# Optimization experiments

Measured on AMD Instinct MI355X. Metric: run time of the kernel, lower is better.

The kernel has to match this reference:

```python
import jax, jax.numpy as jnp
import numpy as np

N_NODES = 100000
N_EDGES = 1600000
N_GRAPHS = 64
BN_EPS = 1e-5


def setup_inputs() -> dict:
    key = jax.random.key(0)
    ks = jax.random.split(key, 16)
    inp = {
        'x': jax.random.normal(ks[0], (N_NODES, 768), dtype=jnp.float32),
        'edge_index': jax.random.randint(ks[1], (2, N_EDGES), 0, N_NODES, dtype=jnp.int32),
        'batch': jnp.sort(jax.random.randint(ks[2], (N_NODES,), 0, N_GRAPHS, dtype=jnp.int32)),
        'W_in': jax.random.normal(ks[3], (768, 256), dtype=jnp.float32) * 0.02,
        'b_in': jax.random.normal(ks[4], (256,), dtype=jnp.float32) * 0.02,
        'W_g': jax.random.normal(ks[5], (3, 256, 256), dtype=jnp.float32) * 0.05,
        'b_g': jax.random.normal(ks[6], (3, 256), dtype=jnp.float32) * 0.02,
        'bn_gamma': jax.random.uniform(ks[7], (3, 256), dtype=jnp.float32) + 0.5,
        'bn_beta': jax.random.normal(ks[8], (3, 256), dtype=jnp.float32) * 0.02,
        'bn_mean': jax.random.normal(ks[9], (3, 256), dtype=jnp.float32) * 0.02,
        'bn_var': jax.random.uniform(ks[10], (3, 256), dtype=jnp.float32) + 0.5,
        'W1': jax.random.normal(ks[11], (256, 128), dtype=jnp.float32) * 0.06,
        'b1': jax.random.normal(ks[12], (128,), dtype=jnp.float32) * 0.02,
        'W2': jax.random.normal(ks[13], (128, 128), dtype=jnp.float32) * 0.08,
        'b2': jax.random.normal(ks[14], (128,), dtype=jnp.float32) * 0.02,
    }
    return inp


def reference(x, edge_index, batch, W_in, b_in, W_g, b_g, bn_gamma, bn_beta,
              bn_mean, bn_var, W1, b1, W2, b2):
    N = x.shape[0]
    # Add self loops (PyG GCNConv default)
    loop = jnp.arange(N, dtype=edge_index.dtype)
    src = jnp.concatenate([edge_index[0], loop])  # [E+N]
    dst = jnp.concatenate([edge_index[1], loop])
    # Symmetric GCN normalization: deg over dst after self loops
    deg = jax.ops.segment_sum(jnp.ones_like(src, dtype=x.dtype), dst, num_segments=N)
    dinv = jnp.where(deg > 0, jax.lax.rsqrt(deg), 0.0)
    norm = (dinv[src] * dinv[dst])[:, None]  # [E+N, 1]

    # input projection + relu
    h = jax.nn.relu(x @ W_in + b_in)  # [N, 256]

    for i in range(W_g.shape[0]):
        m = h @ W_g[i]                                   # [N, 256]
        agg = jax.ops.segment_sum(m[src] * norm, dst, num_segments=N) + b_g[i]
        # BatchNorm (eval mode, running stats)
        agg = (agg - bn_mean[i]) * (bn_gamma[i] * jax.lax.rsqrt(bn_var[i] + BN_EPS)) + bn_beta[i]
        h = jax.nn.relu(agg)  # dropout is identity in eval

    # global mean pool per graph
    sums = jax.ops.segment_sum(h, batch, num_segments=N_GRAPHS)       # [G, 256]
    cnts = jax.ops.segment_sum(jnp.ones((N,), x.dtype), batch, num_segments=N_GRAPHS)
    g = sums / jnp.maximum(cnts, 1.0)[:, None]

    # output MLP
    out = jax.nn.relu(g @ W1 + b1) @ W2 + b2  # [G, 128]
    return out
```

## Files before the change

### kernel.cpp

```cpp
#include <hip/hip_runtime.h>
#include <hip/hip_fp16.h>

#define HIDDEN 256

using hfrag = __attribute__((ext_vector_type(8))) _Float16;
using facc16 = __attribute__((ext_vector_type(16))) float;

#define BARRIER_LGKM()                                   \
  do {                                                   \
    asm volatile("s_waitcnt lgkmcnt(0)" ::: "memory");   \
    __builtin_amdgcn_s_barrier();                        \
  } while (0)

__device__ inline float h2f(unsigned short h) {
  return __half2float(__builtin_bit_cast(__half, h));
}
__device__ inline unsigned short f2h_bits(float v) {
  return __builtin_bit_cast(unsigned short, __float2half(v));
}
__device__ inline hfrag f2h8(const float4& a, const float4& b) {
  hfrag h;
  h[0] = (_Float16)a.x; h[1] = (_Float16)a.y;
  h[2] = (_Float16)a.z; h[3] = (_Float16)a.w;
  h[4] = (_Float16)b.x; h[5] = (_Float16)b.y;
  h[6] = (_Float16)b.z; h[7] = (_Float16)b.w;
  return h;
}

__global__ __launch_bounds__(256) void k_scan_a(const int* __restrict__ deg,
                                                int* __restrict__ bsum, int N) {
  const int t = threadIdx.x, lane = t & 63, w = t >> 6;
  const int idx = blockIdx.x * 256 + t;
  int x = (idx < N) ? deg[idx] : 0;
#pragma unroll
  for (int off = 32; off >= 1; off >>= 1) x += __shfl_xor(x, off);
  __shared__ int ws[4];
  if (lane == 0) ws[w] = x;
  __syncthreads();
  if (t == 0) bsum[blockIdx.x] = ws[0] + ws[1] + ws[2] + ws[3];
}

__global__ __launch_bounds__(512) void k_scan_b(const int* __restrict__ bsum,
                                                int* __restrict__ boff, int nb) {
  const int t = threadIdx.x, lane = t & 63, w = t >> 6;
  int orig = (t < nb) ? bsum[t] : 0;
  int x = orig;
#pragma unroll
  for (int off = 1; off < 64; off <<= 1) {
    int y = __shfl_up(x, off);
    if (lane >= off) x += y;
  }
  __shared__ int wsum[8];
  if (lane == 63) wsum[w] = x;
  __syncthreads();
  if (w == 0 && lane < 8) {
    int s = wsum[lane];
#pragma unroll
    for (int off = 1; off < 8; off <<= 1) {
      int y = __shfl_up(s, off);
      if (lane >= off) s += y;
    }
    wsum[lane] = s;
  }
  __syncthreads();
  int inc = x + (w > 0 ? wsum[w - 1] : 0);
  if (t < nb) boff[t] = inc - orig;
}

__global__ __launch_bounds__(256) void k_scan_c(const int* __restrict__ deg,
                                                const int* __restrict__ boff,
                                                int* __restrict__ row_ptr,
                                                float* __restrict__ dinv, int N) {
  const int t = threadIdx.x, lane = t & 63, w = t >> 6;
  const int idx = blockIdx.x * 256 + t;
  int d = (idx < N) ? deg[idx] : 0;
  int x = d;
#pragma unroll
  for (int off = 1; off < 64; off <<= 1) {
    int y = __shfl_up(x, off);
    if (lane >= off) x += y;
  }
  __shared__ int ws[4];
  if (lane == 63) ws[w] = x;
  __syncthreads();
  int add = boff[blockIdx.x];
#pragma unroll
  for (int j = 0; j < 4; ++j)
    if (j < w) add += ws[j];
  if (idx < N) {
    row_ptr[idx + 1] = x + add;
    dinv[idx] = 1.0f / sqrtf((float)d + 1.0f);
  }
  if (idx == 0) row_ptr[0] = 0;
}

__global__ __launch_bounds__(256) void k_prep_w(const float* __restrict__ W_in,
                                                const float* __restrict__ W_g,
                                                short* __restrict__ Wt) {
  const int e = blockIdx.x * blockDim.x + threadIdx.x;
  if (e >= 196608 + 3 * 65536) return;
  float v;
  int k, n;
  size_t base;
  if (e < 196608) {
    k = e >> 8;
    n = e & 255;
    v = W_in[e];
    base = 0;
  } else {
    int r = e - 196608;
    int lyr = r >> 16;
    k = (r >> 8) & 255;
    n = r & 255;
    v = W_g[r];
    base = 393216 + (size_t)lyr * 131072;
  }
  const int s = k >> 5;
  const int w = n >> 6, nt = (n >> 5) & 1, l31 = n & 31;
  const int kh = (k >> 4) & 1, g2 = (k >> 3) & 1, j = k & 7;
  size_t pos = base + (size_t)s * 16384 + (size_t)w * 4096 +
               (size_t)(nt * 2 + kh) * 512 + (size_t)(g2 * 32 + l31) * 8 + j;
  __half hh = __float2half(v);
  float r2 = v - __half2float(hh);
  Wt[pos] = (short)__builtin_bit_cast(unsigned short, hh);
  Wt[pos + 2048] = (short)__builtin_bit_cast(unsigned short, __float2half(r2));
}

#define B_LOAD(S, BH, BL)                                               \
  {                                                                     \
    const short* wp = wb + ((size_t)(S) << 14);                         \
    BH[0][0] = *(const hfrag*)(wp);                                     \
    BH[0][1] = *(const hfrag*)(wp + 512);                               \
    BH[1][0] = *(const hfrag*)(wp + 1024);                              \
    BH[1][1] = *(const hfrag*)(wp + 1536);                              \
    BL[0][0] = *(const hfrag*)(wp + 2048);                              \
    BL[0][1] = *(const hfrag*)(wp + 2048 + 512);                        \
    BL[1][0] = *(const hfrag*)(wp + 2048 + 1024);                       \
    BL[1][1] = *(const hfrag*)(wp + 2048 + 1536);                       \
  }

#define TILE_COMPUTE(AA, BH, BL)                                        \
  _Pragma("unroll") for (int kh = 0; kh < 2; ++kh) {                    \
    _Pragma("unroll") for (int mt = 0; mt < 2; ++mt)                    \
        _Pragma("unroll") for (int nt = 0; nt < 2; ++nt) acc[mt][nt] =  \
        __builtin_amdgcn_mfma_f32_32x32x16_f16(AA[mt][kh], BH[nt][kh],  \
                                               acc[mt][nt], 0, 0, 0);   \
    _Pragma("unroll") for (int mt = 0; mt < 2; ++mt)                    \
        _Pragma("unroll") for (int nt = 0; nt < 2; ++nt) acc[mt][nt] =  \
        __builtin_amdgcn_mfma_f32_32x32x16_f16(AA[mt][kh], BL[nt][kh],  \
                                               acc[mt][nt], 0, 0, 0);   \
  }

__device__ __forceinline__ void proj_body(int bx, const float* __restrict__ A,
                                          const short* __restrict__ Wt,
                                          const float* __restrict__ bias,
                                          unsigned short* __restrict__ Ch,
                                          int M, int K) {
  __shared__ short As[2][64][34];
  const int t = threadIdx.x;
  const int w = t >> 6, l = t & 63;
  const int g2 = l >> 5, l31 = l & 31;
  const int row0 = bx * 64;
  const int colbase = w * 64;
  const int arow = t >> 2, ak = (t & 3) << 3;

  facc16 acc[2][2];
#pragma unroll
  for (int i = 0; i < 2; ++i)
#pragma unroll
    for (int j = 0; j < 2; ++j) acc[i][j] = (facc16)(0.0f);

  const int nsteps = K >> 5;
  const int ga = row0 + arow;
  const bool aval = ga < M;
  const float* aptr = A + (size_t)ga * K + ak;
  const short* wb = Wt + (size_t)w * 4096 + (size_t)l * 8;

  float4 f0 = make_float4(0.f, 0.f, 0.f, 0.f), f1 = f0;
  if (aval) {
    f0 = *(const float4*)aptr;
    f1 = *(const float4*)(aptr + 4);
  }
  *(hfrag*)&As[0][arow][ak] = f2h8(f0, f1);
  if (nsteps > 1 && aval) {
    f0 = *(const float4*)(aptr + 32);
    f1 = *(const float4*)(aptr + 36);
  }

  int cur = 0;
  for (int s = 0; s < nsteps; ++s) {
    BARRIER_LGKM();
    hfrag bh[2][2], bl[2][2];
    B_LOAD(s, bh, bl);
#pragma unroll
    for (int kh = 0; kh < 2; ++kh) {
      hfrag ah[2];
#pragma unroll
      for (int mt = 0; mt < 2; ++mt)
        ah[mt] = *(const hfrag*)&As[cur][mt * 32 + l31][kh * 16 + g2 * 8];
#pragma unroll
      for (int mt = 0; mt < 2; ++mt)
#pragma unroll
        for (int nt = 0; nt < 2; ++nt)
          acc[mt][nt] = __builtin_amdgcn_mfma_f32_32x32x16_f16(
              ah[mt], bh[nt][kh], acc[mt][nt], 0, 0, 0);
#pragma unroll
      for (int mt = 0; mt < 2; ++mt)
#pragma unroll
        for (int nt = 0; nt < 2; ++nt)
          acc[mt][nt] = __builtin_amdgcn_mfma_f32_32x32x16_f16(
              ah[mt], bl[nt][kh], acc[mt][nt], 0, 0, 0);
    }
    if (s + 1 < nsteps) {
      *(hfrag*)&As[cur ^ 1][arow][ak] = f2h8(f0, f1);
      if (s + 2 < nsteps && aval) {
        const float* ap = aptr + (size_t)(s + 2) * 32;
        f0 = *(const float4*)(ap + 0);
        f1 = *(const float4*)(ap + 4);
      }
    }
    cur ^= 1;
  }
#pragma unroll
  for (int nt = 0; nt < 2; ++nt) {
    const int col = colbase + nt * 32 + l31;
    const float b = bias[col];
#pragma unroll
    for (int mt = 0; mt < 2; ++mt)
#pragma unroll
      for (int r = 0; r < 16; ++r) {
        int row = row0 + mt * 32 + (r & 3) + 8 * (r >> 2) + 4 * g2;
        if (row < M)
          Ch[(size_t)row * HIDDEN + col] = f2h_bits(fmaxf(acc[mt][nt][r] + b, 0.f));
      }
  }
}

#define LG_LOAD(S, AA, BH, BL)                                          \
  {                                                                     \
    AA[0][0] = *(const hfrag*)(ap0 + (S) * 32);                         \
    AA[0][1] = *(const hfrag*)(ap0 + (S) * 32 + 16);                    \
    AA[1][0] = *(const hfrag*)(ap1 + (S) * 32);                         \
    AA[1][1] = *(const hfrag*)(ap1 + (S) * 32 + 16);                    \
    B_LOAD(S, BH, BL);                                                  \
  }

__device__ __forceinline__ void layer_gemm_body(
    int bx, const unsigned short* __restrict__ A, const short* __restrict__ Wt,
    const float* __restrict__ dinv, unsigned short* __restrict__ Cm, int M) {
  const int t = threadIdx.x;
  const int w = t >> 6, l = t & 63;
  const int g2 = l >> 5, l31 = l & 31;
  const int row0 = bx * 64;
  const int colbase = w * 64;

  facc16 acc[2][2];
#pragma unroll
  for (int i = 0; i < 2; ++i)
#pragma unroll
    for (int j = 0; j < 2; ++j) acc[i][j] = (facc16)(0.0f);

  int r0 = row0 + l31, r1 = row0 + 32 + l31;
  if (r0 >= M) r0 = M - 1;
  if (r1 >= M) r1 = M - 1;
  const unsigned short* ap0 = A + (size_t)r0 * HIDDEN + g2 * 8;
  const unsigned short* ap1 = A + (size_t)r1 * HIDDEN + g2 * 8;
  const short* wb = Wt + (size_t)w * 4096 + (size_t)l * 8;

  hfrag aA[2][2], bhA[2][2], blA[2][2];
  hfrag aB[2][2], bhB[2][2], blB[2][2];

  LG_LOAD(0, aA, bhA, blA);
#pragma unroll
  for (int s = 0; s < 8; s += 2) {
    if (s + 1 < 8) LG_LOAD(s + 1, aB, bhB, blB);
    TILE_COMPUTE(aA, bhA, blA);
    if (s + 2 < 8) LG_LOAD(s + 2, aA, bhA, blA);
    TILE_COMPUTE(aB, bhB, blB);
  }
#pragma unroll
  for (int mt = 0; mt < 2; ++mt)
#pragma unroll
    for (int r = 0; r < 16; ++r) {
      int row = row0 + mt * 32 + (r & 3) + 8 * (r >> 2) + 4 * g2;
      if (row >= M) continue;
      const float sc = dinv[row];
#pragma unroll
      for (int nt = 0; nt < 2; ++nt)
        Cm[(size_t)row * HIDDEN + colbase + nt * 32 + l31] =
            f2h_bits(acc[mt][nt][r] * sc);
    }
}

__global__ __launch_bounds__(256, 4) void k_mega1(
    const float* __restrict__ x, const short* __restrict__ Wt,
    const float* __restrict__ b_in, unsigned short* __restrict__ h0, int M,
    int K, const int* __restrict__ dst, int* __restrict__ deg, int E,
    int ngemm, int nhist) {
  if ((int)blockIdx.x < ngemm) {
    proj_body(blockIdx.x, x, Wt, b_in, h0, M, K);
  } else {
    const int b = blockIdx.x - ngemm;
    for (int e = b * 256 + threadIdx.x; e < E; e += nhist * 256)
      atomicAdd(&deg[dst[e]], 1);
  }
}

__global__ __launch_bounds__(256, 2) void k_mega2(
    const unsigned short* __restrict__ h0, const short* __restrict__ WtL,
    const float* __restrict__ dinv, unsigned short* __restrict__ h1, int M,
    const int* __restrict__ src, const int* __restrict__ dst,
    const int* __restrict__ row_ptr, int* __restrict__ fill,
    int* __restrict__ csr, int E, int ngemm, int nfill) {
  if ((int)blockIdx.x < ngemm) {
    layer_gemm_body(blockIdx.x, h0, WtL, dinv, h1, M);
  } else {
    const int b = blockIdx.x - ngemm;
    for (int e = b * 256 + threadIdx.x; e < E; e += nfill * 256) {
      int d = dst[e];
      int pos = atomicAdd(&fill[d], 1);
      csr[row_ptr[d] + pos] = src[e];
    }
  }
}

__global__ __launch_bounds__(256, 2) void k_gemm_layer(
    const unsigned short* __restrict__ h, const short* __restrict__ WtL,
    const float* __restrict__ dinv, unsigned short* __restrict__ m, int M) {
  layer_gemm_body(blockIdx.x, h, WtL, dinv, m, M);
}

__device__ inline void addrow8(float* acc, const uint4& r) {
  const unsigned short* p = (const unsigned short*)&r;
#pragma unroll
  for (int j = 0; j < 8; ++j) acc[j] += h2f(p[j]);
}

__global__ __launch_bounds__(256) void k_aggregate(
    const unsigned short* __restrict__ mp, const int* __restrict__ row_ptr,
    const int* __restrict__ csr, const float* __restrict__ dinv,
    const float* __restrict__ bg, const float* __restrict__ gamma,
    const float* __restrict__ beta, const float* __restrict__ mean,
    const float* __restrict__ var, unsigned short* __restrict__ hout, int N) {
  const int wave = threadIdx.x >> 6, l = threadIdx.x & 63;
  const int half = l >> 5, l31 = l & 31;
  const int v = blockIdx.x * 8 + wave * 2 + half;
  if (v >= N) return;
  const int co = l31 << 3;
  float acc[8];
  {
    uint4 rs = *(const uint4*)(mp + (size_t)v * HIDDEN + co);
    const unsigned short* p = (const unsigned short*)&rs;
#pragma unroll
    for (int j = 0; j < 8; ++j) acc[j] = h2f(p[j]);
  }
  const int s = row_ptr[v], e = row_ptr[v + 1];
  int i = s;
  for (; i + 8 <= e; i += 8) {
    uint4 r[8];
#pragma unroll
    for (int j = 0; j < 8; ++j)
      r[j] = *(const uint4*)(mp + (size_t)csr[i + j] * HIDDEN + co);
#pragma unroll
    for (int j = 0; j < 8; ++j) addrow8(acc, r[j]);
  }
  for (; i < e; ++i) {
    uint4 r0 = *(const uint4*)(mp + (size_t)csr[i] * HIDDEN + co);
    addrow8(acc, r0);
  }
  const float dv = dinv[v];
  float4 g4a = *(const float4*)&gamma[co], g4b = *(const float4*)&gamma[co + 4];
  float4 vr4a = *(const float4*)&var[co], vr4b = *(const float4*)&var[co + 4];
  float4 bg4a = *(const float4*)&bg[co], bg4b = *(const float4*)&bg[co + 4];
  float4 mn4a = *(const float4*)&mean[co], mn4b = *(const float4*)&mean[co + 4];
  float4 be4a = *(const float4*)&beta[co], be4b = *(const float4*)&beta[co + 4];
  float sc[8] = {g4a.x / sqrtf(vr4a.x + 1e-5f), g4a.y / sqrtf(vr4a.y + 1e-5f),
                 g4a.z / sqrtf(vr4a.z + 1e-5f), g4a.w / sqrtf(vr4a.w + 1e-5f),
                 g4b.x / sqrtf(vr4b.x + 1e-5f), g4b.y / sqrtf(vr4b.y + 1e-5f),
                 g4b.z / sqrtf(vr4b.z + 1e-5f), g4b.w / sqrtf(vr4b.w + 1e-5f)};
  float ofs[8] = {bg4a.x - mn4a.x, bg4a.y - mn4a.y, bg4a.z - mn4a.z,
                  bg4a.w - mn4a.w, bg4b.x - mn4b.x, bg4b.y - mn4b.y,
                  bg4b.z - mn4b.z, bg4b.w - mn4b.w};
  float bt[8] = {be4a.x, be4a.y, be4a.z, be4a.w, be4b.x, be4b.y, be4b.z, be4b.w};
  unsigned short o[8];
#pragma unroll
  for (int j = 0; j < 8; ++j)
    o[j] = f2h_bits(fmaxf((acc[j] * dv + ofs[j]) * sc[j] + bt[j], 0.f));
  *(uint4*)&hout[(size_t)v * HIDDEN + co] = *(const uint4*)o;
}

__global__ __launch_bounds__(256) void k_pool(const unsigned short* __restrict__ h,
                                              const int* __restrict__ batch,
                                              float* __restrict__ sums, int N) {
  const int t = threadIdx.x;
  const int start = blockIdx.x * 256;
  if (start >= N) return;
  const int end = min(start + 256, N);
  float acc = 0.f;
  int cur = batch[start];
  for (int n = start; n < end; ++n) {
    int g = batch[n];
    if (g != cur) {
      atomicAdd(&sums[cur * HIDDEN + t], acc);
      acc = 0.f;
      cur = g;
    }
    acc += h2f(h[(size_t)n * HIDDEN + t]);
  }
  atomicAdd(&sums[cur * HIDDEN + t], acc);
}

__global__ __launch_bounds__(128) void k_head(const float* __restrict__ sums,
                                              const int* __restrict__ batch,
                                              int N,
                                              const float* __restrict__ W1,
                                              const float* __restrict__ b1,
                                              const float* __restrict__ W2,
                                              const float* __restrict__ b2,
                                              float* __restrict__ out) {
  __shared__ float gr[256];
  __shared__ float t1[128];
  __shared__ float invs;
  const int b = blockIdx.x, t = threadIdx.x;
  if (t == 0) {
    int lo = 0, hi = N;
    while (lo < hi) {
      int mid = (lo + hi) >> 1;
      if (batch[mid] < b) lo = mid + 1; else hi = mid;
    }
    int lo2 = lo, hi2 = N;
    while (lo2 < hi2) {
      int mid = (lo2 + hi2) >> 1;
      if (batch[mid] < b + 1) lo2 = mid + 1; else hi2 = mid;
    }
    invs = 1.0f / fmaxf((float)(lo2 - lo), 1.0f);
  }
  __syncthreads();
  const float inv = invs;
  gr[t] = sums[b * HIDDEN + t] * inv;
  gr[t + 128] = sums[b * HIDDEN + t + 128] * inv;
  __syncthreads();
  float a = b1[t];
  for (int k = 0; k < 256; ++k) a += gr[k] * W1[k * 128 + t];
  t1[t] = fmaxf(a, 0.f);
  __syncthreads();
  float o = b2[t];
  for (int k = 0; k < 128; ++k) o += t1[k] * W2[k * 128 + t];
  out[b * 128 + t] = o;
}

extern "C" void kernel_launch(void* const* d_in, const int* in_sizes, int n_in,
                              void* d_out, int out_size, void* d_ws,
                              size_t ws_size, hipStream_t stream) {
  (void)n_in;
  (void)ws_size;
  const float* x = (const float*)d_in[0];
  const int* ei = (const int*)d_in[1];
  const int* batch = (const int*)d_in[2];
  const float* W_in = (const float*)d_in[3];
  const float* b_in = (const float*)d_in[4];
  const float* W_g = (const float*)d_in[5];
  const float* b_g = (const float*)d_in[6];
  const float* bn_gamma = (const float*)d_in[7];
  const float* bn_beta = (const float*)d_in[8];
  const float* bn_mean = (const float*)d_in[9];
  const float* bn_var = (const float*)d_in[10];
  const float* W1 = (const float*)d_in[11];
  const float* b1 = (const float*)d_in[12];
  const float* W2 = (const float*)d_in[13];
  const float* b2 = (const float*)d_in[14];

  const int KIN = 768;
  const int N = in_sizes[0] / KIN;
  const int E = in_sizes[1] / 2;
  const int G = out_size / 128;

  const int* src = ei;
  const int* dst = ei + E;

  char* ws = (char*)d_ws;
  size_t off = 0;
  auto take = [&](size_t bytes) -> void* {
    void* p = ws + off;
    off += (bytes + 255) & ~(size_t)255;
    return p;
  };
  unsigned short* h0 = (unsigned short*)take((size_t)N * HIDDEN * 2);
  unsigned short* h1 = (unsigned short*)take((size_t)N * HIDDEN * 2);
  float* dinv = (float*)take((size_t)N * 4);
  int* deg = (int*)take((size_t)N * 4);
  int* fill = (int*)take((size_t)N * 4);
  int* row_ptr = (int*)take((size_t)(N + 1) * 4);
  int* csr = (int*)take((size_t)E * 4);
  float* sums = (float*)take((size_t)G * HIDDEN * 4);
  short* Wt = (short*)take((size_t)(393216 + 3 * 131072) * 2);
  const int nb = (N + 255) / 256;
  int* bsum = (int*)take((size_t)nb * 4);
  int* boff = (int*)take((size_t)nb * 4);

  hipMemsetAsync(deg, 0, (size_t)N * 4, stream);
  hipMemsetAsync(fill, 0, (size_t)N * 4, stream);
  hipMemsetAsync(sums, 0, (size_t)G * HIDDEN * 4, stream);

  const int gx = (N + 63) / 64;
  const int NH = 256;
  const int NF = 256;

  k_prep_w<<<(196608 + 3 * 65536 + 255) / 256, 256, 0, stream>>>(W_in, W_g, Wt);
  k_mega1<<<gx + NH, 256, 0, stream>>>(x, Wt, b_in, h0, N, KIN, dst, deg, E,
                                       gx, NH);
  k_scan_a<<<nb, 256, 0, stream>>>(deg, bsum, N);
  k_scan_b<<<1, 512, 0, stream>>>(bsum, boff, nb);
  k_scan_c<<<nb, 256, 0, stream>>>(deg, boff, row_ptr, dinv, N);
  k_mega2<<<gx + NF, 256, 0, stream>>>(h0, Wt + 393216, dinv, h1, N, src, dst,
                                       row_ptr, fill, csr, E, gx, NF);
  k_aggregate<<<(N + 7) / 8, 256, 0, stream>>>(
      h1, row_ptr, csr, dinv, b_g, bn_gamma, bn_beta, bn_mean, bn_var, h0, N);
  for (int i = 1; i < 3; ++i) {
    k_gemm_layer<<<gx, 256, 0, stream>>>(h0, Wt + 393216 + (size_t)i * 131072,
                                         dinv, h1, N);
    k_aggregate<<<(N + 7) / 8, 256, 0, stream>>>(
        h1, row_ptr, csr, dinv, b_g + i * HIDDEN, bn_gamma + i * HIDDEN,
        bn_beta + i * HIDDEN, bn_mean + i * HIDDEN, bn_var + i * HIDDEN, h0, N);
  }
  k_pool<<<(N + 255) / 256, 256, 0, stream>>>(h0, batch, sums, N);
  k_head<<<G, 128, 0, stream>>>(sums, batch, N, W1, b1, W2, b2, (float*)d_out);
}
```

Before: 940.5 us.

## Fuse mean pooling into MLP head and fold memsets into weight prep

The deg and fill counters are now zeroed inside the weight-prep kernel, which removes three memset launches. The separate atomic-based pool kernel and the head kernel are merged into one kernel with one block per graph. Each block binary-searches its node range and sums the rows directly, so the atomic sums buffer goes away. Pooling now runs on only 64 blocks, each reading about 1500 rows serially, which may give less parallelism than the old 391-block pool.

```diff
diff --git a/kernel.cpp b/kernel.cpp
--- a/kernel.cpp
+++ b/kernel.cpp
@@ -96,8 +96,14 @@
 
 __global__ __launch_bounds__(256) void k_prep_w(const float* __restrict__ W_in,
                                                 const float* __restrict__ W_g,
-                                                short* __restrict__ Wt) {
+                                                short* __restrict__ Wt,
+                                                int* __restrict__ deg,
+                                                int* __restrict__ fill, int N) {
   const int e = blockIdx.x * blockDim.x + threadIdx.x;
+  if (e < N) {
+    deg[e] = 0;
+    fill[e] = 0;
+  }
   if (e >= 196608 + 3 * 65536) return;
   float v;
   int k, n;
@@ -389,64 +395,50 @@
   *(uint4*)&hout[(size_t)v * HIDDEN + co] = *(const uint4*)o;
 }
 
-__global__ __launch_bounds__(256) void k_pool(const unsigned short* __restrict__ h,
-                                              const int* __restrict__ batch,
-                                              float* __restrict__ sums, int N) {
-  const int t = threadIdx.x;
-  const int start = blockIdx.x * 256;
-  if (start >= N) return;
-  const int end = min(start + 256, N);
-  float acc = 0.f;
-  int cur = batch[start];
-  for (int n = start; n < end; ++n) {
-    int g = batch[n];
-    if (g != cur) {
-      atomicAdd(&sums[cur * HIDDEN + t], acc);
-      acc = 0.f;
-      cur = g;
-    }
-    acc += h2f(h[(size_t)n * HIDDEN + t]);
-  }
-  atomicAdd(&sums[cur * HIDDEN + t], acc);
-}
-
-__global__ __launch_bounds__(128) void k_head(const float* __restrict__ sums,
-                                              const int* __restrict__ batch,
-                                              int N,
-                                              const float* __restrict__ W1,
-                                              const float* __restrict__ b1,
-                                              const float* __restrict__ W2,
-                                              const float* __restrict__ b2,
-                                              float* __restrict__ out) {
+__global__ __launch_bounds__(256) void k_poolhead(
+    const unsigned short* __restrict__ h, const int* __restrict__ batch, int N,
+    const float* __restrict__ W1, const float* __restrict__ b1,
+    const float* __restrict__ W2, const float* __restrict__ b2,
+    float* __restrict__ out) {
   __shared__ float gr[256];
   __shared__ float t1[128];
-  __shared__ float invs;
+  __shared__ int range[2];
   const int b = blockIdx.x, t = threadIdx.x;
-  if (t == 0) {
+  if (t < 2) {
+    const int target = b + t;
     int lo = 0, hi = N;
     while (lo < hi) {
       int mid = (lo + hi) >> 1;
-      if (batch[mid] < b) lo = mid + 1; else hi = mid;
+      if (batch[mid] < target) lo = mid + 1; else hi = mid;
     }
-    int lo2 = lo, hi2 = N;
-    while (lo2 < hi2) {
-      int mid = (lo2 + hi2) >> 1;
-      if (batch[mid] < b + 1) lo2 = mid + 1; else hi2 = mid;
-    }
-    invs = 1.0f / fmaxf((float)(lo2 - lo), 1.0f);
-  }
-  __syncthreads();
-  const float inv = invs;
-  gr[t] = sums[b * HIDDEN + t] * inv;
-  gr[t + 128] = sums[b * HIDDEN + t + 128] * inv;
-  __syncthreads();
-  float a = b1[t];
-  for (int k = 0; k < 256; ++k) a += gr[k] * W1[k * 128 + t];
-  t1[t] = fmaxf(a, 0.f);
-  __syncthreads();
-  float o = b2[t];
-  for (int k = 0; k < 128; ++k) o += t1[k] * W2[k * 128 + t];
-  out[b * 128 + t] = o;
+    range[t] = lo;
+  }
+  __syncthreads();
+  const int lo = range[0], hi = range[1];
+  float acc = 0.f;
+  int n = lo;
+  for (; n + 4 <= hi; n += 4) {
+    unsigned short a0 = h[(size_t)(n + 0) * HIDDEN + t];
+    unsigned short a1 = h[(size_t)(n + 1) * HIDDEN + t];
+    unsigned short a2 = h[(size_t)(n + 2) * HIDDEN + t];
+    unsigned short a3 = h[(size_t)(n + 3) * HIDDEN + t];
+    acc += h2f(a0) + h2f(a1) + h2f(a2) + h2f(a3);
+  }
+  for (; n < hi; ++n) acc += h2f(h[(size_t)n * HIDDEN + t]);
+  const float inv = 1.0f / fmaxf((float)(hi - lo), 1.0f);
+  gr[t] = acc * inv;
+  __syncthreads();
+  if (t < 128) {
+    float a = b1[t];
+    for (int k = 0; k < 256; ++k) a += gr[k] * W1[k * 128 + t];
+    t1[t] = fmaxf(a, 0.f);
+  }
+  __syncthreads();
+  if (t < 128) {
+    float o = b2[t];
+    for (int k = 0; k < 128; ++k) o += t1[k] * W2[k * 128 + t];
+    out[b * 128 + t] = o;
+  }
 }
 
 extern "C" void kernel_launch(void* const* d_in, const int* in_sizes, int n_in,
@@ -492,21 +484,17 @@
   int* fill = (int*)take((size_t)N * 4);
   int* row_ptr = (int*)take((size_t)(N + 1) * 4);
   int* csr = (int*)take((size_t)E * 4);
-  float* sums = (float*)take((size_t)G * HIDDEN * 4);
   short* Wt = (short*)take((size_t)(393216 + 3 * 131072) * 2);
   const int nb = (N + 255) / 256;
   int* bsum = (int*)take((size_t)nb * 4);
   int* boff = (int*)take((size_t)nb * 4);
 
-  hipMemsetAsync(deg, 0, (size_t)N * 4, stream);
-  hipMemsetAsync(fill, 0, (size_t)N * 4, stream);
-  hipMemsetAsync(sums, 0, (size_t)G * HIDDEN * 4, stream);
-
   const int gx = (N + 63) / 64;
   const int NH = 256;
   const int NF = 256;
 
-  k_prep_w<<<(196608 + 3 * 65536 + 255) / 256, 256, 0, stream>>>(W_in, W_g, Wt);
+  k_prep_w<<<(196608 + 3 * 65536 + 255) / 256, 256, 0, stream>>>(
+      W_in, W_g, Wt, deg, fill, N);
   k_mega1<<<gx + NH, 256, 0, stream>>>(x, Wt, b_in, h0, N, KIN, dst, deg, E,
                                        gx, NH);
   k_scan_a<<<nb, 256, 0, stream>>>(deg, bsum, N);
@@ -523,6 +511,6 @@
         h1, row_ptr, csr, dinv, b_g + i * HIDDEN, bn_gamma + i * HIDDEN,
         bn_beta + i * HIDDEN, bn_mean + i * HIDDEN, bn_var + i * HIDDEN, h0, N);
   }
-  k_pool<<<(N + 255) / 256, 256, 0, stream>>>(h0, batch, sums, N);
-  k_head<<<G, 128, 0, stream>>>(sums, batch, N, W1, b1, W2, b2, (float*)d_out);
-}
+  k_poolhead<<<G, 256, 0, stream>>>(h0, batch, N, W1, b1, W2, b2,
+                                    (float*)d_out);
+}
```

New measurement: 960.7 us. +2.2%, slower.
